# Kernel optimization log

Hardware: AMD Instinct MI355X
Metric: run time of the kernel (lower is better)

The kernel has to match this reference:

```python
import jax, jax.numpy as jnp
import numpy as np

B, T, I, H, C = 128, 512, 256, 1024, 1000

def setup_inputs() -> dict:
    key = jax.random.key(0)
    ks = jax.random.split(key, 7)
    s_ih = 1.0 / np.sqrt(H)
    return {
        "x": jax.random.normal(ks[0], (B, T, I), dtype=jnp.float32),
        "W_ih": jax.random.normal(ks[1], (4 * H, I), dtype=jnp.float32) * s_ih,
        "W_hh": jax.random.normal(ks[2], (4 * H, H), dtype=jnp.float32) * s_ih,
        "b_ih": jax.random.normal(ks[3], (4 * H,), dtype=jnp.float32) * s_ih,
        "b_hh": jax.random.normal(ks[4], (4 * H,), dtype=jnp.float32) * s_ih,
        "fc_W": jax.random.normal(ks[5], (C, H), dtype=jnp.float32) * s_ih,
        "fc_b": jax.random.normal(ks[6], (C,), dtype=jnp.float32) * s_ih,
    }

def _lstm_scan(x, W_ih, W_hh, b_ih, b_hh):
    # Precompute input projections for all timesteps in one big GEMM: [T, B, 4H]
    xg = jnp.einsum('bti,gi->tbg', x, W_ih) + b_ih

    def step(carry, xg_t):
        h, c = carry
        gates = xg_t + h @ W_hh.T + b_hh          # [B, 4H]
        i, f, g, o = jnp.split(gates, 4, axis=-1)  # PyTorch LSTMCell gate order
        i = jax.nn.sigmoid(i)
        f = jax.nn.sigmoid(f)
        g = jnp.tanh(g)
        o = jax.nn.sigmoid(o)
        c = f * c + i * g
        h = o * jnp.tanh(c)
        return (h, c), None

    h0 = jnp.zeros((x.shape[0], W_hh.shape[1]), dtype=x.dtype)
    (h, c), _ = jax.lax.scan(step, (h0, h0), xg)
    return h

def reference(x, W_ih, W_hh, b_ih, b_hh, fc_W, fc_b):
    h = _lstm_scan(x, W_ih, W_hh, b_ih, b_hh)  # final hidden state [B, H]
    return h @ fc_W.T + fc_b                   # [B, C]
```

## Files before the change

### kernel.cpp

```cpp
#include <hip/hip_runtime.h>
#include <hip/hip_bf16.h>

#define B_DIM 128
#define T_DIM 512
#define I_DIMV 256
#define H_DIM 1024
#define G_DIM 4096
#define K_TOT 1280
#define C_DIM 1000
#define A_STRIDE 1288

typedef __attribute__((ext_vector_type(8))) short short8;
typedef __attribute__((ext_vector_type(4))) float f32x4;
typedef __attribute__((ext_vector_type(4))) unsigned short ushort4v;
typedef __attribute__((ext_vector_type(4))) int int4v;

__device__ __forceinline__ unsigned short f2bf(float f) {
    unsigned int u = __float_as_uint(f);
    u += 0x7FFF + ((u >> 16) & 1);
    return (unsigned short)(u >> 16);
}

__device__ __forceinline__ float sigmoid_f(float x) {
    return __builtin_amdgcn_rcpf(1.0f + __expf(-x));
}
__device__ __forceinline__ float tanh_f(float x) {
    return 1.0f - 2.0f * __builtin_amdgcn_rcpf(1.0f + __expf(2.0f * x));
}

__global__ void prep_kernel(const float* __restrict__ x,
                            const float* __restrict__ Wih,
                            const float* __restrict__ Whh,
                            const float* __restrict__ bih,
                            const float* __restrict__ bhh,
                            unsigned short* __restrict__ Wc,
                            unsigned short* __restrict__ xbf,
                            float* __restrict__ biasc,
                            unsigned short* __restrict__ h0,
                            unsigned* __restrict__ bar)
{
    const int tid = blockIdx.x * blockDim.x + threadIdx.x;
    const int nth = gridDim.x * blockDim.x;

    const int WcN4 = G_DIM * K_TOT / 4;
    for (int i = tid; i < WcN4; i += nth) {
        int p = i / (K_TOT / 4);
        int k = (i - p * (K_TOT / 4)) * 4;
        int j = p >> 2, q = p & 3;
        int r = q * H_DIM + j;
        const float* src = (k < H_DIM) ? (Whh + (size_t)r * H_DIM + k)
                                       : (Wih + (size_t)r * I_DIMV + (k - H_DIM));
        f32x4 v = *(const f32x4*)src;
        ushort4v o;
        o.x = f2bf(v.x); o.y = f2bf(v.y); o.z = f2bf(v.z); o.w = f2bf(v.w);
        *(ushort4v*)(Wc + (size_t)i * 4) = o;
    }
    const int xN4 = B_DIM * T_DIM * I_DIMV / 4;
    for (int i = tid; i < xN4; i += nth) {
        f32x4 v = *(const f32x4*)(x + (size_t)i * 4);
        ushort4v o;
        o.x = f2bf(v.x); o.y = f2bf(v.y); o.z = f2bf(v.z); o.w = f2bf(v.w);
        *(ushort4v*)(xbf + (size_t)i * 4) = o;
    }
    for (int p = tid; p < G_DIM; p += nth) {
        int j = p >> 2, q = p & 3;
        int r = q * H_DIM + j;
        biasc[p] = bih[r] + bhh[r];
    }
    const int hN4 = B_DIM * H_DIM / 4;
    for (int i = tid; i < hN4; i += nth) {
        ushort4v z = {0, 0, 0, 0};
        *(ushort4v*)(h0 + (size_t)i * 4) = z;
    }
    for (int i = tid; i < 2048; i += nth) bar[i] = 0;
}

__global__ __launch_bounds__(256, 1)
void lstm_grid(const unsigned short* __restrict__ Wc,
               const unsigned short* __restrict__ xbf,
               const float* __restrict__ biasc,
               unsigned short* __restrict__ hb0,
               unsigned short* __restrict__ hb1,
               float* __restrict__ hf32,
               unsigned* __restrict__ bar)
{
    __shared__ __align__(16) unsigned short Alds[16 * A_STRIDE];

    const int tid   = threadIdx.x;
    const int wgid  = blockIdx.x;
    const int m_blk = wgid >> 5;
    const int n_blk = wgid & 31;
    const int b0 = m_blk * 16;
    const int p0 = n_blk * 128;
    const int j0 = n_blk * 32;

    const int wid  = tid >> 6;
    const int lane = tid & 63;
    const int cl   = lane & 15;
    const int quad = lane >> 4;
    const int q_g  = cl & 3;
    const int jl   = cl >> 2;

    const float bias0 = biasc[p0 + wid * 32 + cl];
    const float bias1 = biasc[p0 + wid * 32 + 16 + cl];

    short8 Wreg[80];
    {
        const unsigned short* w0 = Wc + (size_t)(p0 + wid * 32 + cl) * K_TOT + quad * 8;
        const unsigned short* w1 = w0 + (size_t)16 * K_TOT;
        #pragma unroll
        for (int c = 0; c < 40; ++c) {
            Wreg[c]      = *(const short8*)(w0 + c * 32);
            Wreg[40 + c] = *(const short8*)(w1 + c * 32);
        }
    }

    unsigned* const flags    = bar + 256 * m_blk;
    unsigned* const own_flag = flags + n_blk;

    float c0v = 0.0f, c1v = 0.0f;

    f32x4 xacc0 = {0.f, 0.f, 0.f, 0.f};
    f32x4 xacc1 = {0.f, 0.f, 0.f, 0.f};
    {
        #pragma unroll
        for (int u = 0; u < 2; ++u) {
            const int idx = u * 256 + tid;
            const int row = idx >> 5;
            const int col = (idx & 31) * 8;
            short8 xv = *(const short8*)(xbf + (size_t)(b0 + row) * (T_DIM * I_DIMV)
                                         + col);
            *(short8*)(&Alds[row * A_STRIDE + 1024 + col]) = xv;
        }
        __syncthreads();
        #pragma unroll
        for (int c = 0; c < 8; ++c) {
            short8 a = *(const short8*)(&Alds[cl * A_STRIDE + 1024 + c * 32 + quad * 8]);
            xacc0 = __builtin_amdgcn_mfma_f32_16x16x32_bf16(a, Wreg[32 + c], xacc0, 0, 0, 0);
            xacc1 = __builtin_amdgcn_mfma_f32_16x16x32_bf16(a, Wreg[72 + c], xacc1, 0, 0, 0);
        }
    }

    const int colh = lane * 8;

    for (int t = 0; t < T_DIM; ++t) {
        const unsigned short* hread = (t & 1) ? hb1 : hb0;
        unsigned short* hwrite      = (t & 1) ? hb0 : hb1;

        if (t > 0) {
            while (true) {
                unsigned v = 0xFFFFFFFFu;
                if (lane < 32) {
                    const unsigned* p = flags + lane;
                    asm volatile("global_load_dword %0, %1, off sc0 sc1"
                                 : "=v"(v) : "v"(p) : "memory");
                    asm volatile("s_waitcnt vmcnt(0)" ::: "memory");
                }
                if (__ballot(v >= (unsigned)t) == ~0ull) break;
                __builtin_amdgcn_s_sleep(1);
            }
        }

        int4v htA[4], htB[4];
        #pragma unroll
        for (int u = 0; u < 4; ++u) {
            const int row = u * 4 + wid;
            const unsigned short* src = hread + (size_t)(b0 + row) * H_DIM + colh;
            asm volatile("global_load_dwordx4 %0, %1, off sc0 sc1"
                         : "=v"(htA[u]) : "v"(src) : "memory");
        }
        #pragma unroll
        for (int u = 0; u < 4; ++u) {
            const int row = u * 4 + wid;
            const unsigned short* src = hread + (size_t)(b0 + row) * H_DIM + 512 + colh;
            asm volatile("global_load_dwordx4 %0, %1, off sc0 sc1"
                         : "=v"(htB[u]) : "v"(src) : "memory");
        }
        asm volatile("s_waitcnt vmcnt(4)" ::: "memory");
        #pragma unroll
        for (int u = 0; u < 4; ++u) {
            *(int4v*)(&Alds[(u * 4 + wid) * A_STRIDE + colh]) = htA[u];
        }
        __syncthreads();

        f32x4 acc0 = xacc0;
        f32x4 acc1 = xacc1;
        #pragma unroll
        for (int c = 0; c < 16; ++c) {
            short8 a = *(const short8*)(&Alds[cl * A_STRIDE + c * 32 + quad * 8]);
            acc0 = __builtin_amdgcn_mfma_f32_16x16x32_bf16(a, Wreg[c],      acc0, 0, 0, 0);
            acc1 = __builtin_amdgcn_mfma_f32_16x16x32_bf16(a, Wreg[40 + c], acc1, 0, 0, 0);
        }

        asm volatile("s_waitcnt vmcnt(0)" ::: "memory");
        #pragma unroll
        for (int u = 0; u < 4; ++u) {
            *(int4v*)(&Alds[(u * 4 + wid) * A_STRIDE + 512 + colh]) = htB[u];
        }
        __syncthreads();

        #pragma unroll
        for (int c = 16; c < 32; ++c) {
            short8 a = *(const short8*)(&Alds[cl * A_STRIDE + c * 32 + quad * 8]);
            acc0 = __builtin_amdgcn_mfma_f32_16x16x32_bf16(a, Wreg[c],      acc0, 0, 0, 0);
            acc1 = __builtin_amdgcn_mfma_f32_16x16x32_bf16(a, Wreg[40 + c], acc1, 0, 0, 0);
        }

        float hn[2];
        #pragma unroll
        for (int s = 0; s < 2; ++s) {
            const f32x4 accv = s ? acc1 : acc0;
            const float bs   = s ? bias1 : bias0;
            float e[4];
            #pragma unroll
            for (int r = 0; r < 4; ++r) e[r] = accv[r] + bs;
            float t1[4];
            #pragma unroll
            for (int r = 0; r < 4; ++r) t1[r] = __shfl_xor(e[r ^ 1], 1);
            #pragma unroll
            for (int r = 0; r < 4; ++r) e[r] = ((q_g ^ r) & 1) ? t1[r] : e[r];
            float t2[4];
            #pragma unroll
            for (int r = 0; r < 4; ++r) t2[r] = __shfl_xor(e[r ^ 2], 2);
            #pragma unroll
            for (int r = 0; r < 4; ++r) e[r] = ((q_g ^ r) & 2) ? t2[r] : e[r];

            const float ig = sigmoid_f(e[0]);
            const float fg = sigmoid_f(e[1]);
            const float gg = tanh_f(e[2]);
            const float og = sigmoid_f(e[3]);
            const float cp = s ? c1v : c0v;
            const float cn = fg * cp + ig * gg;
            if (s) c1v = cn; else c0v = cn;
            hn[s] = og * tanh_f(cn);
        }

        const unsigned short hb16_0 = f2bf(hn[0]);
        const unsigned short hb16_1 = f2bf(hn[1]);
        unsigned p32_0 = (unsigned)hb16_0 |
            ((unsigned)(unsigned short)__shfl_xor((int)hb16_0, 4) << 16);
        unsigned p32_1 = (unsigned)hb16_1 |
            ((unsigned)(unsigned short)__shfl_xor((int)hb16_1, 4) << 16);
        unsigned hi_0 = (unsigned)__shfl_xor((int)p32_0, 8);
        unsigned hi_1 = (unsigned)__shfl_xor((int)p32_1, 8);

        const int brow = quad * 4 + q_g;
        if (jl == 0 && t + 1 < T_DIM) {
            int4v val;
            val.x = (int)p32_0; val.y = (int)hi_0;
            val.z = (int)p32_1; val.w = (int)hi_1;
            unsigned short* dst =
                hwrite + (size_t)(b0 + brow) * H_DIM + j0 + wid * 8;
            asm volatile("global_store_dwordx4 %0, %1, off sc0 sc1"
                         :: "v"(dst), "v"(val) : "memory");
        }
        if (t == T_DIM - 1) {
            const size_t base = (size_t)(b0 + brow) * H_DIM + j0 + wid * 8 + jl;
            hf32[base]     = hn[0];
            hf32[base + 4] = hn[1];
        }

        if (t + 1 < T_DIM) {
            __syncthreads();
            if (tid == 0) {
                unsigned e = (unsigned)(t + 1);
                asm volatile("global_store_dword %0, %1, off sc0 sc1"
                             :: "v"(own_flag), "v"(e) : "memory");
            }
            #pragma unroll
            for (int u = 0; u < 2; ++u) {
                const int idx = u * 256 + tid;
                const int row = idx >> 5;
                const int col = (idx & 31) * 8;
                short8 xv = *(const short8*)(xbf + (size_t)(b0 + row) * (T_DIM * I_DIMV)
                                             + (size_t)(t + 1) * I_DIMV + col);
                *(short8*)(&Alds[row * A_STRIDE + 1024 + col]) = xv;
            }
            __syncthreads();
            xacc0 = (f32x4){0.f, 0.f, 0.f, 0.f};
            xacc1 = (f32x4){0.f, 0.f, 0.f, 0.f};
            #pragma unroll
            for (int c = 0; c < 8; ++c) {
                short8 a = *(const short8*)(&Alds[cl * A_STRIDE + 1024 + c * 32 + quad * 8]);
                xacc0 = __builtin_amdgcn_mfma_f32_16x16x32_bf16(a, Wreg[32 + c], xacc0, 0, 0, 0);
                xacc1 = __builtin_amdgcn_mfma_f32_16x16x32_bf16(a, Wreg[72 + c], xacc1, 0, 0, 0);
            }
        }
    }
}

__global__ __launch_bounds__(256)
void fc_kernel(const float* __restrict__ hf32,
               const float* __restrict__ fcW,
               const float* __restrict__ fcb,
               float* __restrict__ out)
{
    __shared__ __align__(16) float hs[16 * 256];
    const int tid = threadIdx.x;
    const int b0 = blockIdx.x * 16;
    const int o0 = blockIdx.y * 64;
    const int to = tid & 63;
    const int tb = tid >> 6;
    const int o  = o0 + to;
    const bool active = (o < C_DIM);

    float acc[4] = {0.f, 0.f, 0.f, 0.f};

    for (int jc = 0; jc < H_DIM; jc += 256) {
        __syncthreads();
        {
            const int row = tid >> 4;
            const int c0  = (tid & 15) * 16;
            #pragma unroll
            for (int u = 0; u < 4; ++u) {
                *(f32x4*)(&hs[row * 256 + c0 + u * 4]) =
                    *(const f32x4*)(hf32 + (size_t)(b0 + row) * H_DIM + jc + c0 + u * 4);
            }
        }
        __syncthreads();
        if (active) {
            for (int j4 = 0; j4 < 256; j4 += 4) {
                f32x4 wv = *(const f32x4*)(fcW + (size_t)o * H_DIM + jc + j4);
                #pragma unroll
                for (int bb = 0; bb < 4; ++bb) {
                    f32x4 hv = *(const f32x4*)(&hs[(tb * 4 + bb) * 256 + j4]);
                    acc[bb] += wv.x * hv.x + wv.y * hv.y + wv.z * hv.z + wv.w * hv.w;
                }
            }
        }
    }
    if (active) {
        const float bias = fcb[o];
        #pragma unroll
        for (int bb = 0; bb < 4; ++bb) {
            out[(size_t)(b0 + tb * 4 + bb) * C_DIM + o] = acc[bb] + bias;
        }
    }
}

extern "C" void kernel_launch(void* const* d_in, const int* in_sizes, int n_in,
                              void* d_out, int out_size, void* d_ws, size_t ws_size,
                              hipStream_t stream)
{
    const float* x   = (const float*)d_in[0];
    const float* Wih = (const float*)d_in[1];
    const float* Whh = (const float*)d_in[2];
    const float* bih = (const float*)d_in[3];
    const float* bhh = (const float*)d_in[4];
    const float* fcW = (const float*)d_in[5];
    const float* fcb = (const float*)d_in[6];
    float* out = (float*)d_out;

    char* ws = (char*)d_ws;
    unsigned short* Wc  = (unsigned short*)(ws + 0);
    unsigned short* xbf = (unsigned short*)(ws + 10485760);
    float* biasc        = (float*)(ws + 44040192);
    unsigned short* hb0 = (unsigned short*)(ws + 44056576);
    unsigned short* hb1 = (unsigned short*)(ws + 44318720);
    float* hf32         = (float*)(ws + 44580864);
    unsigned* bar       = (unsigned*)d_out;

    hipLaunchKernelGGL(prep_kernel, dim3(1024), dim3(256), 0, stream,
                       x, Wih, Whh, bih, bhh, Wc, xbf, biasc, hb0, bar);

    hipLaunchKernelGGL(lstm_grid, dim3(256), dim3(256), 0, stream,
                       Wc, xbf, biasc, hb0, hb1, hf32, bar);

    hipLaunchKernelGGL(fc_kernel, dim3(8, 16), dim3(256), 0, stream,
                       hf32, fcW, fcb, out);
}
```

Baseline: 2.006 ms.

## Co-locate batch groups on one XCD and use L2-scope coherence when verified

Remaps workgroup IDs so the 32 workgroups sharing a batch block are spaced by 8, which under round-robin XCD dispatch is meant to place them on the same XCD. A startup handshake writes per-workgroup magic values with L2-scope stores and checks that all peers see them; if so, flag polling, hidden-state loads and stores use sc0-only (L2-coherent) instead of sc0 sc1 system-scope accesses, avoiding trips past L2. It falls back to the old system-scope path if the check fails, at the cost of an extra barrier at startup and a dependency on the dispatch-to-XCD mapping.

```diff
diff --git a/kernel.cpp b/kernel.cpp
--- a/kernel.cpp
+++ b/kernel.cpp
@@ -72,7 +72,7 @@
         ushort4v z = {0, 0, 0, 0};
         *(ushort4v*)(h0 + (size_t)i * 4) = z;
     }
-    for (int i = tid; i < 2048; i += nth) bar[i] = 0;
+    for (int i = tid; i < 4096; i += nth) bar[i] = 0;
 }
 
 __global__ __launch_bounds__(256, 1)
@@ -88,8 +88,8 @@
 
     const int tid   = threadIdx.x;
     const int wgid  = blockIdx.x;
-    const int m_blk = wgid >> 5;
-    const int n_blk = wgid & 31;
+    const int m_blk = wgid & 7;
+    const int n_blk = wgid >> 3;
     const int b0 = m_blk * 16;
     const int p0 = n_blk * 128;
     const int j0 = n_blk * 32;
@@ -117,6 +117,45 @@
 
     unsigned* const flags    = bar + 256 * m_blk;
     unsigned* const own_flag = flags + n_blk;
+    unsigned* const pready   = bar + 2048 + 256 * m_blk;
+    unsigned* const pmagic   = pready + 32;
+
+    bool l2path;
+    {
+        const unsigned mymagic = 0x5EED0000u | (unsigned)wgid;
+        if (tid == 0) {
+            unsigned* p = pmagic + n_blk;
+            asm volatile("global_store_dword %0, %1, off sc0"
+                         :: "v"(p), "v"(mymagic) : "memory");
+        }
+        __syncthreads();
+        if (tid == 0) {
+            unsigned one = 1u;
+            unsigned* p = pready + n_blk;
+            asm volatile("global_store_dword %0, %1, off sc0 sc1"
+                         :: "v"(p), "v"(one) : "memory");
+        }
+        while (true) {
+            unsigned v = 1u;
+            if (lane < 32) {
+                const unsigned* p = pready + lane;
+                asm volatile("global_load_dword %0, %1, off sc0 sc1"
+                             : "=v"(v) : "v"(p) : "memory");
+                asm volatile("s_waitcnt vmcnt(0)" ::: "memory");
+            }
+            if (__ballot(v >= 1u) == ~0ull) break;
+            __builtin_amdgcn_s_sleep(1);
+        }
+        unsigned expect = 0x5EED0000u | (unsigned)((lane << 3) | m_blk);
+        unsigned got = expect;
+        if (lane < 32) {
+            const unsigned* p = pmagic + lane;
+            asm volatile("global_load_dword %0, %1, off sc0"
+                         : "=v"(got) : "v"(p) : "memory");
+            asm volatile("s_waitcnt vmcnt(0)" ::: "memory");
+        }
+        l2path = (__ballot(got == expect) == ~0ull);
+    }
 
     float c0v = 0.0f, c1v = 0.0f;
 
@@ -148,33 +187,64 @@
         unsigned short* hwrite      = (t & 1) ? hb0 : hb1;
 
         if (t > 0) {
-            while (true) {
-                unsigned v = 0xFFFFFFFFu;
-                if (lane < 32) {
-                    const unsigned* p = flags + lane;
-                    asm volatile("global_load_dword %0, %1, off sc0 sc1"
-                                 : "=v"(v) : "v"(p) : "memory");
-                    asm volatile("s_waitcnt vmcnt(0)" ::: "memory");
+            if (l2path) {
+                while (true) {
+                    unsigned v = 0xFFFFFFFFu;
+                    if (lane < 32) {
+                        const unsigned* p = flags + lane;
+                        asm volatile("global_load_dword %0, %1, off sc0"
+                                     : "=v"(v) : "v"(p) : "memory");
+                        asm volatile("s_waitcnt vmcnt(0)" ::: "memory");
+                    }
+                    if (__ballot(v >= (unsigned)t) == ~0ull) break;
+                    __builtin_amdgcn_s_sleep(1);
                 }
-                if (__ballot(v >= (unsigned)t) == ~0ull) break;
-                __builtin_amdgcn_s_sleep(1);
+            } else {
+                while (true) {
+                    unsigned v = 0xFFFFFFFFu;
+                    if (lane < 32) {
+                        const unsigned* p = flags + lane;
+                        asm volatile("global_load_dword %0, %1, off sc0 sc1"
+                                     : "=v"(v) : "v"(p) : "memory");
+                        asm volatile("s_waitcnt vmcnt(0)" ::: "memory");
+                    }
+                    if (__ballot(v >= (unsigned)t) == ~0ull) break;
+                    __builtin_amdgcn_s_sleep(1);
+                }
             }
         }
 
         int4v htA[4], htB[4];
-        #pragma unroll
-        for (int u = 0; u < 4; ++u) {
-            const int row = u * 4 + wid;
-            const unsigned short* src = hread + (size_t)(b0 + row) * H_DIM + colh;
-            asm volatile("global_load_dwordx4 %0, %1, off sc0 sc1"
-                         : "=v"(htA[u]) : "v"(src) : "memory");
-        }
-        #pragma unroll
-        for (int u = 0; u < 4; ++u) {
-            const int row = u * 4 + wid;
-            const unsigned short* src = hread + (size_t)(b0 + row) * H_DIM + 512 + colh;
-            asm volatile("global_load_dwordx4 %0, %1, off sc0 sc1"
-                         : "=v"(htB[u]) : "v"(src) : "memory");
+        if (l2path) {
+            #pragma unroll
+            for (int u = 0; u < 4; ++u) {
+                const unsigned short* src =
+                    hread + (size_t)(b0 + u * 4 + wid) * H_DIM + colh;
+                asm volatile("global_load_dwordx4 %0, %1, off sc0"
+                             : "=v"(htA[u]) : "v"(src) : "memory");
+            }
+            #pragma unroll
+            for (int u = 0; u < 4; ++u) {
+                const unsigned short* src =
+                    hread + (size_t)(b0 + u * 4 + wid) * H_DIM + 512 + colh;
+                asm volatile("global_load_dwordx4 %0, %1, off sc0"
+                             : "=v"(htB[u]) : "v"(src) : "memory");
+            }
+        } else {
+            #pragma unroll
+            for (int u = 0; u < 4; ++u) {
+                const unsigned short* src =
+                    hread + (size_t)(b0 + u * 4 + wid) * H_DIM + colh;
+                asm volatile("global_load_dwordx4 %0, %1, off sc0 sc1"
+                             : "=v"(htA[u]) : "v"(src) : "memory");
+            }
+            #pragma unroll
+            for (int u = 0; u < 4; ++u) {
+                const unsigned short* src =
+                    hread + (size_t)(b0 + u * 4 + wid) * H_DIM + 512 + colh;
+                asm volatile("global_load_dwordx4 %0, %1, off sc0 sc1"
+                             : "=v"(htB[u]) : "v"(src) : "memory");
+            }
         }
         asm volatile("s_waitcnt vmcnt(4)" ::: "memory");
         #pragma unroll
@@ -251,8 +321,13 @@
             val.z = (int)p32_1; val.w = (int)hi_1;
             unsigned short* dst =
                 hwrite + (size_t)(b0 + brow) * H_DIM + j0 + wid * 8;
-            asm volatile("global_store_dwordx4 %0, %1, off sc0 sc1"
-                         :: "v"(dst), "v"(val) : "memory");
+            if (l2path) {
+                asm volatile("global_store_dwordx4 %0, %1, off sc0"
+                             :: "v"(dst), "v"(val) : "memory");
+            } else {
+                asm volatile("global_store_dwordx4 %0, %1, off sc0 sc1"
+                             :: "v"(dst), "v"(val) : "memory");
+            }
         }
         if (t == T_DIM - 1) {
             const size_t base = (size_t)(b0 + brow) * H_DIM + j0 + wid * 8 + jl;
@@ -264,8 +339,13 @@
             __syncthreads();
             if (tid == 0) {
                 unsigned e = (unsigned)(t + 1);
-                asm volatile("global_store_dword %0, %1, off sc0 sc1"
-                             :: "v"(own_flag), "v"(e) : "memory");
+                if (l2path) {
+                    asm volatile("global_store_dword %0, %1, off sc0"
+                                 :: "v"(own_flag), "v"(e) : "memory");
+                } else {
+                    asm volatile("global_store_dword %0, %1, off sc0 sc1"
+                                 :: "v"(own_flag), "v"(e) : "memory");
+                }
             }
             #pragma unroll
             for (int u = 0; u < 2; ++u) {
```

Measured after the change: 1.721 ms. 1.17x faster.
